# Kernel tuning notes

Hardware: AMD Instinct MI355X
Metric: run time of the kernel (lower is better)

The kernel has to match this reference:

```python
import jax, jax.numpy as jnp
import numpy as np

N_BCH = 8        # molecules per batch
N_ATM = 10000    # atoms per molecule
N_EDGE = 5_120_000  # ~avg degree 64
N_ELM = 100      # element-type table size


def setup_inputs() -> dict:
    key = jax.random.key(0)
    k1, k2, k3, k4, k5, k6, k7 = jax.random.split(key, 7)
    elm = jax.random.randint(k1, (N_BCH, N_ATM), 0, N_ELM)
    edge_n = jax.random.randint(k2, (N_EDGE,), 0, N_BCH)
    edge_i = jax.random.randint(k3, (N_EDGE,), 0, N_ATM)
    edge_j = jax.random.randint(k4, (N_EDGE,), 0, N_ATM)
    # squared distances in [0, 4) -> dis in [0, 2)
    sod = jax.random.uniform(k5, (N_EDGE,), dtype=jnp.float32) * 4.0
    # per-element force constant and radius (positive)
    k_param = jax.random.uniform(k6, (N_ELM,), dtype=jnp.float32) + 0.5
    radius = jax.random.uniform(k7, (N_ELM,), dtype=jnp.float32) * 0.5 + 0.5
    return {"elm": elm, "edge_n": edge_n, "edge_i": edge_i, "edge_j": edge_j,
            "sod": sod, "k": k_param, "radius": radius}


def reference(elm, edge_n, edge_i, edge_j, sod, k, radius):
    # gather per-edge element types
    ei = elm[edge_n, edge_i]          # [E]
    ej = elm[edge_n, edge_j]          # [E]
    dis = jnp.sqrt(sod)               # [E]
    kk = k[ei] + k[ej]                # [E]
    R = radius[ei] + radius[ej]       # [E]
    mask = dis < R
    d = dis - R
    eng_bnd = jnp.where(mask, kk * d * d, jnp.zeros((), dtype=sod.dtype))  # [E]
    # scatter-add per atom: flat index n*n_atm + i
    seg = edge_n * N_ATM + edge_i
    eng_atm = jax.ops.segment_sum(eng_bnd, seg, num_segments=N_BCH * N_ATM)
    eng_atm = eng_atm.reshape(N_BCH, N_ATM)
    eng_mol = eng_atm.sum(axis=1)     # [n_bch]
    return eng_mol
```

## Files before the change

kernel.cpp:

```cpp
#include <hip/hip_runtime.h>
#include <hip/hip_bf16.h>

#define N_BCH 8
#define N_ATM 10000
#define N_ELM 100
#define N_ATOMS_TOT (N_BCH * N_ATM)

typedef int   i4 __attribute__((ext_vector_type(4)));
typedef float f4 __attribute__((ext_vector_type(4)));

__launch_bounds__(256)
__global__ void pack_elm_kernel(const int* __restrict__ elm,
                                unsigned int* __restrict__ elm_u8_as_u32,
                                float* __restrict__ out) {
    int t = blockIdx.x * blockDim.x + threadIdx.x;
    if (t < N_ATOMS_TOT / 4) {
        i4 v = *(const i4*)(elm + 4 * t);
        unsigned int packed = (unsigned int)(v[0] & 0xff)
                            | ((unsigned int)(v[1] & 0xff) << 8)
                            | ((unsigned int)(v[2] & 0xff) << 16)
                            | ((unsigned int)(v[3] & 0xff) << 24);
        elm_u8_as_u32[t] = packed;
    }
    if (blockIdx.x == 0 && threadIdx.x < N_BCH) out[threadIdx.x] = 0.0f;
}

__launch_bounds__(512, 4)
__global__ void edge_kernel(const unsigned int* __restrict__ elm_u8,
                            const float* __restrict__ kparam,
                            const float* __restrict__ radius,
                            const int* __restrict__ edge_n,
                            const int* __restrict__ edge_i,
                            const int* __restrict__ edge_j,
                            const float* __restrict__ sod,
                            float* __restrict__ out,
                            int nE) {
    __shared__ unsigned int s_elm32[N_ATOMS_TOT / 4];
    __shared__ float s_kr[256];
    __shared__ float s_red[8][N_BCH];

    {
        const i4* src = (const i4*)elm_u8;
        i4* dst = (i4*)s_elm32;
        for (int t = threadIdx.x; t < N_ATOMS_TOT / 16; t += 512)
            dst[t] = src[t];
        if (threadIdx.x < N_ELM) {
            s_kr[threadIdx.x]       = kparam[threadIdx.x];
            s_kr[128 + threadIdx.x] = radius[threadIdx.x];
        }
    }
    __syncthreads();

    const unsigned char* s_elm = (const unsigned char*)s_elm32;

    float acc[N_BCH];
#pragma unroll
    for (int b = 0; b < N_BCH; ++b) acc[b] = 0.0f;

    const int tid    = blockIdx.x * blockDim.x + threadIdx.x;
    const int stride = gridDim.x * blockDim.x;
    const int nvec   = nE >> 2;

    const i4* en4 = (const i4*)edge_n;
    const i4* ei4 = (const i4*)edge_i;
    const i4* ej4 = (const i4*)edge_j;
    const f4* s4  = (const f4*)sod;

    for (int v = tid; v < nvec; v += stride) {
        i4 nn = __builtin_nontemporal_load(en4 + v);
        i4 ii = __builtin_nontemporal_load(ei4 + v);
        i4 jj = __builtin_nontemporal_load(ej4 + v);
        f4 ss = __builtin_nontemporal_load(s4  + v);

#pragma unroll
        for (int u = 0; u < 4; ++u) {
            int base = nn[u] * N_ATM;
            int ei = s_elm[base + ii[u]];
            int ej = s_elm[base + jj[u]];
            float ki = s_kr[ei], ri = s_kr[128 + ei];
            float kj = s_kr[ej], rj = s_kr[128 + ej];
            float dis = __builtin_amdgcn_sqrtf(ss[u]);
            float kk = ki + kj;
            float R  = ri + rj;
            float d  = dis - R;
            float val = (dis < R) ? kk * d * d : 0.0f;
            int n = nn[u];
#pragma unroll
            for (int b = 0; b < N_BCH; ++b)
                acc[b] += (n == b) ? val : 0.0f;
        }
    }

    const int tail_start = nvec << 2;
    const int tail_n = nE - tail_start;
    if (tid < tail_n) {
        int e = tail_start + tid;
        int n = edge_n[e];
        int ei = s_elm[n * N_ATM + edge_i[e]];
        int ej = s_elm[n * N_ATM + edge_j[e]];
        float dis = __builtin_amdgcn_sqrtf(sod[e]);
        float kk = s_kr[ei] + s_kr[ej];
        float R  = s_kr[128 + ei] + s_kr[128 + ej];
        float d  = dis - R;
        float val = (dis < R) ? kk * d * d : 0.0f;
#pragma unroll
        for (int b = 0; b < N_BCH; ++b)
            acc[b] += (n == b) ? val : 0.0f;
    }

#pragma unroll
    for (int b = 0; b < N_BCH; ++b) {
        float x = acc[b];
#pragma unroll
        for (int off = 32; off > 0; off >>= 1)
            x += __shfl_down(x, off, 64);
        acc[b] = x;
    }

    const int wave = threadIdx.x >> 6;
    const int lane = threadIdx.x & 63;
    if (lane == 0) {
#pragma unroll
        for (int b = 0; b < N_BCH; ++b) s_red[wave][b] = acc[b];
    }
    __syncthreads();
    if (threadIdx.x < N_BCH) {
        float x = 0.0f;
#pragma unroll
        for (int w = 0; w < 8; ++w) x += s_red[w][threadIdx.x];
        atomicAdd(&out[threadIdx.x], x);
    }
}

extern "C" void kernel_launch(void* const* d_in, const int* in_sizes, int n_in,
                              void* d_out, int out_size, void* d_ws, size_t ws_size,
                              hipStream_t stream) {
    const int*   elm    = (const int*)d_in[0];
    const int*   edge_n = (const int*)d_in[1];
    const int*   edge_i = (const int*)d_in[2];
    const int*   edge_j = (const int*)d_in[3];
    const float* sod    = (const float*)d_in[4];
    const float* kparam = (const float*)d_in[5];
    const float* radius = (const float*)d_in[6];
    float* out = (float*)d_out;
    const int nE = in_sizes[1];

    unsigned int* elm_u8 = (unsigned int*)d_ws;

    hipLaunchKernelGGL(pack_elm_kernel, dim3((N_ATOMS_TOT / 4 + 255) / 256),
                       dim3(256), 0, stream, elm, elm_u8, out);
    hipLaunchKernelGGL(edge_kernel, dim3(512), dim3(512), 0, stream,
                       elm_u8, kparam, radius, edge_n, edge_i, edge_j, sod,
                       out, nE);
}
```

Baseline: 127.9 us.

## Pack k/radius as half2, use 1024-thread blocks, and transpose the wave reduction

Stores k and radius together as one half2 entry per element type, so each atom's parameters come from a single LDS load and are summed with one packed add. Doubles the block size to 1024 threads with a higher occupancy hint. Replaces the per-batch shuffle-down reduction with an xor-butterfly transpose that needs fewer shuffles. Storing parameters in half precision lowers the accuracy of kk and R and may breach the tolerance; the launch bound of 1024 threads with 8 waves per EU also restricts register use.

```diff
diff --git a/kernel.cpp b/kernel.cpp
--- a/kernel.cpp
+++ b/kernel.cpp
@@ -1,5 +1,6 @@
 #include <hip/hip_runtime.h>
 #include <hip/hip_bf16.h>
+#include <hip/hip_fp16.h>
 
 #define N_BCH 8
 #define N_ATM 10000
@@ -25,7 +26,7 @@
     if (blockIdx.x == 0 && threadIdx.x < N_BCH) out[threadIdx.x] = 0.0f;
 }
 
-__launch_bounds__(512, 4)
+__launch_bounds__(1024, 8)
 __global__ void edge_kernel(const unsigned int* __restrict__ elm_u8,
                             const float* __restrict__ kparam,
                             const float* __restrict__ radius,
@@ -36,18 +37,17 @@
                             float* __restrict__ out,
                             int nE) {
     __shared__ unsigned int s_elm32[N_ATOMS_TOT / 4];
-    __shared__ float s_kr[256];
-    __shared__ float s_red[8][N_BCH];
+    __shared__ __half2 s_kr[128];
+    __shared__ float s_red[16][N_BCH];
 
     {
         const i4* src = (const i4*)elm_u8;
         i4* dst = (i4*)s_elm32;
-        for (int t = threadIdx.x; t < N_ATOMS_TOT / 16; t += 512)
+        for (int t = threadIdx.x; t < N_ATOMS_TOT / 16; t += 1024)
             dst[t] = src[t];
-        if (threadIdx.x < N_ELM) {
-            s_kr[threadIdx.x]       = kparam[threadIdx.x];
-            s_kr[128 + threadIdx.x] = radius[threadIdx.x];
-        }
+        if (threadIdx.x < N_ELM)
+            s_kr[threadIdx.x] =
+                __floats2half2_rn(kparam[threadIdx.x], radius[threadIdx.x]);
     }
     __syncthreads();
 
@@ -74,17 +74,16 @@
 
 #pragma unroll
         for (int u = 0; u < 4; ++u) {
-            int base = nn[u] * N_ATM;
-            int ei = s_elm[base + ii[u]];
-            int ej = s_elm[base + jj[u]];
-            float ki = s_kr[ei], ri = s_kr[128 + ei];
-            float kj = s_kr[ej], rj = s_kr[128 + ej];
-            float dis = __builtin_amdgcn_sqrtf(ss[u]);
-            float kk = ki + kj;
-            float R  = ri + rj;
+            int n = nn[u];
+            int base = n * N_ATM;
+            int e_i = s_elm[base + ii[u]];
+            int e_j = s_elm[base + jj[u]];
+            __half2 krsum = __hadd2(s_kr[e_i], s_kr[e_j]);
+            float kk = __low2float(krsum);
+            float R  = __high2float(krsum);
+            float dis = sqrtf(ss[u]);
             float d  = dis - R;
             float val = (dis < R) ? kk * d * d : 0.0f;
-            int n = nn[u];
 #pragma unroll
             for (int b = 0; b < N_BCH; ++b)
                 acc[b] += (n == b) ? val : 0.0f;
@@ -96,11 +95,12 @@
     if (tid < tail_n) {
         int e = tail_start + tid;
         int n = edge_n[e];
-        int ei = s_elm[n * N_ATM + edge_i[e]];
-        int ej = s_elm[n * N_ATM + edge_j[e]];
-        float dis = __builtin_amdgcn_sqrtf(sod[e]);
-        float kk = s_kr[ei] + s_kr[ej];
-        float R  = s_kr[128 + ei] + s_kr[128 + ej];
+        int e_i = s_elm[n * N_ATM + edge_i[e]];
+        int e_j = s_elm[n * N_ATM + edge_j[e]];
+        __half2 krsum = __hadd2(s_kr[e_i], s_kr[e_j]);
+        float kk = __low2float(krsum);
+        float R  = __high2float(krsum);
+        float dis = sqrtf(sod[e]);
         float d  = dis - R;
         float val = (dis < R) ? kk * d * d : 0.0f;
 #pragma unroll
@@ -108,27 +108,30 @@
             acc[b] += (n == b) ? val : 0.0f;
     }
 
+    const int lane = threadIdx.x & 63;
+    const int wave = threadIdx.x >> 6;
+
 #pragma unroll
-    for (int b = 0; b < N_BCH; ++b) {
-        float x = acc[b];
+    for (int off = 8; off <= 32; off <<= 1) {
 #pragma unroll
-        for (int off = 32; off > 0; off >>= 1)
-            x += __shfl_down(x, off, 64);
-        acc[b] = x;
+        for (int b = 0; b < N_BCH; ++b)
+            acc[b] += __shfl_xor(acc[b], off, 64);
     }
+    const int j = lane >> 3;
+    float x = acc[0];
+#pragma unroll
+    for (int b = 1; b < N_BCH; ++b) x = (j == b) ? acc[b] : x;
+#pragma unroll
+    for (int off = 1; off <= 4; off <<= 1)
+        x += __shfl_xor(x, off, 64);
 
-    const int wave = threadIdx.x >> 6;
-    const int lane = threadIdx.x & 63;
-    if (lane == 0) {
-#pragma unroll
-        for (int b = 0; b < N_BCH; ++b) s_red[wave][b] = acc[b];
-    }
+    if ((lane & 7) == 0) s_red[wave][j] = x;
     __syncthreads();
     if (threadIdx.x < N_BCH) {
-        float x = 0.0f;
+        float v = 0.0f;
 #pragma unroll
-        for (int w = 0; w < 8; ++w) x += s_red[w][threadIdx.x];
-        atomicAdd(&out[threadIdx.x], x);
+        for (int w = 0; w < 16; ++w) v += s_red[w][threadIdx.x];
+        atomicAdd(&out[threadIdx.x], v);
     }
 }
 
@@ -149,7 +152,7 @@
 
     hipLaunchKernelGGL(pack_elm_kernel, dim3((N_ATOMS_TOT / 4 + 255) / 256),
                        dim3(256), 0, stream, elm, elm_u8, out);
-    hipLaunchKernelGGL(edge_kernel, dim3(512), dim3(512), 0, stream,
+    hipLaunchKernelGGL(edge_kernel, dim3(512), dim3(1024), 0, stream,
                        elm_u8, kparam, radius, edge_n, edge_i, edge_j, sod,
                        out, nE);
 }
```

Result: no change. 126.2 us (-1.4%).
